# Optimization experiments

Measured on AMD Instinct MI355X. Metric: run time of the kernel, lower is better.

The kernel has to match this reference:

```python
import jax, jax.numpy as jnp
import numpy as np

B, N, C = 8, 2048, 128
K = 16
DILATIONS = (1, 2)
KMAX = K * max(DILATIONS)  # neighbors constructed by DilatedKnnGraph
NEG_SLOPE = 0.2


def setup_inputs() -> dict:
    key = jax.random.key(0)
    ks = jax.random.split(key, 12)
    D = len(DILATIONS)

    def nrm(k, shape, fan_in):
        return jax.random.normal(k, shape, jnp.float32) / np.float32(np.sqrt(fan_in))

    x = jax.random.normal(ks[0], (B, N, C), jnp.float32)
    pos = jax.random.normal(ks[1], (B, N, 3), jnp.float32)
    # PointTransformerConv params per dilation layer (bias-free lin/lin_src/lin_dst, pos_nn=Linear(3,C))
    W_lin = nrm(ks[2], (D, C, C), C)
    W_src = nrm(ks[3], (D, C, C), C)
    W_dst = nrm(ks[4], (D, C, C), C)
    W_pos = nrm(ks[5], (D, 3, C), 3)
    b_pos = jnp.zeros((D, C), jnp.float32)
    # global fusion MLP: Linear(C+3, C) + LeakyReLU(0.2)
    Wg = nrm(ks[6], (C + 3, C), C + 3)
    bg = jnp.zeros((C,), jnp.float32)
    # final MLP: Linear(C,C) + LeakyReLU(0.2) + Linear(C,3)
    W1 = nrm(ks[7], (C, C), C)
    b1 = jnp.zeros((C,), jnp.float32)
    W2 = nrm(ks[8], (C, 3), C)
    b2 = jnp.zeros((3,), jnp.float32)
    return dict(x=x, pos=pos, W_lin=W_lin, W_src=W_src, W_dst=W_dst,
                W_pos=W_pos, b_pos=b_pos, Wg=Wg, bg=bg, W1=W1, b1=b1, W2=W2, b2=b2)


def _knn(p):
    # p: [N, 3] -> [N, KMAX] neighbor indices sorted by ascending distance (self excluded)
    sq = jnp.sum(p * p, axis=-1)
    d2 = sq[:, None] + sq[None, :] - 2.0 * (p @ p.T)
    d2 = d2 + jnp.eye(p.shape[0], dtype=p.dtype) * jnp.float32(1e10)
    _, idx = jax.lax.top_k(-d2, KMAX)
    return idx


def reference(x, pos, W_lin, W_src, W_dst, W_pos, b_pos, Wg, bg, W1, b1, W2, b2):
    nbr = jax.vmap(_knn)(pos)  # [B, N, KMAX]
    self_idx = jnp.broadcast_to(jnp.arange(N)[None, :, None], (B, N, 1))
    gather = jax.vmap(lambda arr, idx: arr[idx])  # per-cloud fancy gather

    h = None
    for li, d in enumerate(DILATIONS):
        # Dilated neighbor selection: every d-th of sorted neighbors, keep K, plus self loop
        idx = jnp.concatenate([nbr[:, :, ::d][:, :, :K], self_idx], axis=-1)  # [B, N, K+1]
        pos_j = gather(pos, idx)  # [B, N, K+1, 3]
        # delta_ij = pos_nn(pos_i - pos_j)
        delta = jnp.einsum('bnkt,tc->bnkc', pos[:, :, None, :] - pos_j, W_pos[li]) + b_pos[li]
        s = x @ W_src[li]   # lin_src
        v = x @ W_lin[li]   # value projection
        t = x @ W_dst[li]   # lin_dst
        # alpha_ij = lin_dst(x_i) - lin_src(x_j) + delta ; per-channel softmax over neighbors
        alpha = t[:, :, None, :] - gather(s, idx) + delta  # [B, N, K+1, C]
        w = jax.nn.softmax(alpha, axis=2)
        h_ = jnp.sum(w * (gather(v, idx) + delta), axis=2)  # [B, N, C]
        h = h_ if h is None else h + h_

    h2 = jax.nn.leaky_relu(jnp.concatenate([x, pos], axis=-1) @ Wg + bg, NEG_SLOPE)
    h = h + h2
    res = jax.nn.leaky_relu(h @ W1 + b1, NEG_SLOPE) @ W2 + b2
    return res + pos  # add_points=True
```

## Files before the change

### kernel.cpp

```cpp
#include <hip/hip_runtime.h>

#define BB 8
#define NN 2048
#define CC 128
#define KMAX 32
#define NEG 0.2f
#define CH 8
#define CHSZ (NN / CH)
#define CPAD4 257
#define CAP 32

using bf16x8 = __attribute__((ext_vector_type(8))) short;
using f32x4  = __attribute__((ext_vector_type(4))) float;

__device__ __forceinline__ unsigned int f2key(float f) {
  unsigned int b = __float_as_uint(f);
  return (b & 0x80000000u) ? ~b : (b | 0x80000000u);
}

__device__ __forceinline__ float sq3(float x, float y, float z) {
  return __fadd_rn(__fadd_rn(__fmul_rn(x, x), __fmul_rn(y, y)), __fmul_rn(z, z));
}

__device__ __forceinline__ float d2np(float px, float py, float pz, float sqq,
                                      float qx, float qy, float qz, float sqj) {
  float dot = __fmaf_rn(pz, qz, __fmaf_rn(py, qy, __fmul_rn(px, qx)));
  return __fsub_rn(__fadd_rn(sqq, sqj), __fmul_rn(2.0f, dot));
}

__device__ __forceinline__ unsigned short f2bf(float f) {
  unsigned int u = __float_as_uint(f);
  return (unsigned short)((u + 0x7fffu + ((u >> 16) & 1u)) >> 16);
}
__device__ __forceinline__ float bf2f(unsigned short u) {
  return __uint_as_float(((unsigned int)u) << 16);
}

__device__ __forceinline__ bf16x8 cvt8(const float* __restrict__ p) {
  float4 a = *(const float4*)(p);
  float4 b = *(const float4*)(p + 4);
  bf16x8 r;
  r[0] = (short)f2bf(a.x); r[1] = (short)f2bf(a.y);
  r[2] = (short)f2bf(a.z); r[3] = (short)f2bf(a.w);
  r[4] = (short)f2bf(b.x); r[5] = (short)f2bf(b.y);
  r[6] = (short)f2bf(b.z); r[7] = (short)f2bf(b.w);
  return r;
}

__device__ __forceinline__ void proj_body(int z, int mx, int tid,
                                          const float* __restrict__ x,
                                          const unsigned short* __restrict__ wf,
                                          unsigned short* __restrict__ projb) {
  unsigned short* out = projb + (size_t)z * ((size_t)BB * NN * CC);
  int wave = tid >> 6;
  int lane = tid & 63;
  int m0 = (mx * 4 + wave) * 16;
  int quad = lane >> 4;
  int am = m0 + (lane & 15);

  f32x4 acc[8];
#pragma unroll
  for (int nt = 0; nt < 8; ++nt) acc[nt] = (f32x4){0.f, 0.f, 0.f, 0.f};

  const unsigned short* wz = wf + (size_t)z * (8 * 4 * 64 * 8);
#pragma unroll
  for (int ks = 0; ks < 4; ++ks) {
    bf16x8 a = cvt8(x + (size_t)am * CC + ks * 32 + quad * 8);
#pragma unroll
    for (int nt = 0; nt < 8; ++nt) {
      bf16x8 bfr = *(const bf16x8*)(wz + (size_t)(((nt * 4 + ks) * 64 + lane) * 8));
      acc[nt] = __builtin_amdgcn_mfma_f32_16x16x32_bf16(a, bfr, acc[nt], 0, 0, 0);
    }
  }

  int col0 = lane & 15;
#pragma unroll
  for (int nt = 0; nt < 8; ++nt)
#pragma unroll
    for (int r = 0; r < 4; ++r)
      out[(size_t)(m0 + quad * 4 + r) * CC + nt * 16 + col0] = f2bf(acc[nt][r]);
}

__device__ __forceinline__ void wg_body(int mx, int tid,
                                        const float* __restrict__ x,
                                        const float* __restrict__ pos,
                                        const unsigned short* __restrict__ wf,
                                        const float* __restrict__ wgtail,
                                        const float* __restrict__ bg,
                                        float* __restrict__ h) {
  int wave = tid >> 6;
  int lane = tid & 63;
  int m0 = (mx * 4 + wave) * 16;
  int quad = lane >> 4;
  int am = m0 + (lane & 15);

  f32x4 acc[8];
#pragma unroll
  for (int nt = 0; nt < 8; ++nt) acc[nt] = (f32x4){0.f, 0.f, 0.f, 0.f};

  const unsigned short* wz = wf + (size_t)6 * (8 * 4 * 64 * 8);
#pragma unroll
  for (int ks = 0; ks < 4; ++ks) {
    bf16x8 a = cvt8(x + (size_t)am * CC + ks * 32 + quad * 8);
#pragma unroll
    for (int nt = 0; nt < 8; ++nt) {
      bf16x8 b = *(const bf16x8*)(wz + (size_t)(((nt * 4 + ks) * 64 + lane) * 8));
      acc[nt] = __builtin_amdgcn_mfma_f32_16x16x32_bf16(a, b, acc[nt], 0, 0, 0);
    }
  }

  float posr[4][3];
#pragma unroll
  for (int r = 0; r < 4; ++r) {
    int m = m0 + quad * 4 + r;
    posr[r][0] = pos[m * 3 + 0];
    posr[r][1] = pos[m * 3 + 1];
    posr[r][2] = pos[m * 3 + 2];
  }

  int col0 = lane & 15;
#pragma unroll
  for (int nt = 0; nt < 8; ++nt) {
    int col = nt * 16 + col0;
    float bv = bg[col];
    float t0 = wgtail[col];
    float t1 = wgtail[CC + col];
    float t2 = wgtail[2 * CC + col];
#pragma unroll
    for (int r = 0; r < 4; ++r) {
      float v = acc[nt][r] + bv
              + posr[r][0] * t0 + posr[r][1] * t1 + posr[r][2] * t2;
      v = v > 0.f ? v : NEG * v;
      h[(size_t)(m0 + quad * 4 + r) * CC + col] = v;
    }
  }
}

__global__ __launch_bounds__(256) void fused_front(
    const float* __restrict__ pos,
    unsigned short* __restrict__ cand,
    unsigned int* __restrict__ candk,
    const float* __restrict__ x,
    const unsigned short* __restrict__ wf,
    unsigned short* __restrict__ projb,
    const float* __restrict__ wgtail,
    const float* __restrict__ bg,
    float* __restrict__ h) {
  __shared__ float4 sp4[CH * CPAD4];
  __shared__ unsigned int sred[256];
  __shared__ unsigned short sbuf[256 * CAP];

  if (blockIdx.x < 512) {
    int b = blockIdx.x >> 6;
    int qbase = (blockIdx.x & 63) * 32;
    const float* pb = pos + (size_t)b * NN * 3;
    for (int t = threadIdx.x; t < NN; t += 256) {
      int a = ((t >> 8) * CPAD4) + (t & 255);
      float xx = pb[t * 3 + 0];
      float yy = pb[t * 3 + 1];
      float zz = pb[t * 3 + 2];
      sp4[a] = make_float4(xx, yy, zz, sq3(xx, yy, zz));
    }
    __syncthreads();

    int q = qbase + (threadIdx.x >> 3);
    int c = threadIdx.x & 7;
    int qa = ((q >> 8) * CPAD4) + (q & 255);
    float4 pq = sp4[qa];
    float px = pq.x, py = pq.y, pz = pq.z;
    float sqq = pq.w;

    int abase = c * CPAD4;
    int j0 = c * CHSZ;

    unsigned int a0 = 0xFFFFFFFFu, a1 = 0xFFFFFFFFu, a2 = 0xFFFFFFFFu, a3 = 0xFFFFFFFFu;
    for (int jj = 0; jj < CHSZ; ++jj) {
      int j = j0 + jj;
      float4 pj = sp4[abase + jj];
      float d2 = d2np(px, py, pz, sqq, pj.x, pj.y, pj.z, pj.w);
      unsigned int key = f2key(d2);
      if (j == q) key = 0xFFFFFFFFu;
      if (key < a3) {
        bool c3 = key < a2;
        a3 = c3 ? a2 : key;
        bool c2 = key < a1;
        a2 = c3 ? (c2 ? a1 : key) : a2;
        bool c1 = key < a0;
        a1 = c2 ? (c1 ? a0 : key) : a1;
        a0 = c1 ? key : a0;
      }
    }
    sred[threadIdx.x] = a3;
    __syncthreads();
    if (c == 0) {
      unsigned int m = sred[threadIdx.x];
#pragma unroll
      for (int u = 1; u < 8; ++u) {
        unsigned int v = sred[threadIdx.x + u];
        m = v > m ? v : m;
      }
      sred[threadIdx.x] = m;
    }
    __syncthreads();
    unsigned int T = sred[threadIdx.x & ~7];

    unsigned int ak[KMAX];
    int ai[KMAX];
#pragma unroll
    for (int k = 0; k < KMAX; ++k) { ak[k] = 0xFFFFFFFFu; ai[k] = 0xFFFF; }

    int sbase = threadIdx.x * CAP;
    auto drain = [&](int cnt2) {
      for (int u = 0; u < cnt2; ++u) {
        int jj2 = (int)sbuf[sbase + u];
        int j = j0 + jj2;
        float4 pj = sp4[abase + jj2];
        float d2 = d2np(px, py, pz, sqq, pj.x, pj.y, pj.z, pj.w);
        unsigned int key = f2key(d2);
        if (key < ak[KMAX - 1]) {
#pragma unroll
          for (int k = KMAX - 1; k >= 1; --k) {
            bool ck  = key < ak[k];
            bool ckm = key < ak[k - 1];
            unsigned int tk = ckm ? ak[k - 1] : key;
            int          ti = ckm ? ai[k - 1] : j;
            ak[k] = ck ? tk : ak[k];
            ai[k] = ck ? ti : ai[k];
          }
          bool c0b = key < ak[0];
          ak[0] = c0b ? key : ak[0];
          ai[0] = c0b ? j : ai[0];
        }
      }
    };

    int cnt = 0;
    for (int jj = 0; jj < CHSZ; ++jj) {
      int j = j0 + jj;
      float4 pj = sp4[abase + jj];
      float d2 = d2np(px, py, pz, sqq, pj.x, pj.y, pj.z, pj.w);
      unsigned int key = f2key(d2);
      if (j == q) key = 0xFFFFFFFFu;
      if (key <= T) {
        if (cnt == CAP) { drain(CAP); cnt = 0; }
        sbuf[sbase + cnt] = (unsigned short)jj;
        ++cnt;
      }
    }
    drain(cnt);

    size_t obase = (((size_t)(b * NN + q)) * CH + c) * KMAX;
    unsigned short* oc = cand + obase;
    unsigned int* ok = candk + obase;
#pragma unroll
    for (int k = 0; k < KMAX; ++k) {
      oc[k] = (unsigned short)ai[k];
      ok[k] = ak[k];
    }
  } else if (blockIdx.x < 2048) {
    int bx = blockIdx.x - 512;
    proj_body(bx >> 8, bx & 255, threadIdx.x, x, wf, projb);
  } else {
    wg_body(blockIdx.x - 2048, threadIdx.x, x, pos, wf, wgtail, bg, h);
  }
}

__global__ __launch_bounds__(256) void knn_p1(const float* __restrict__ pos,
                                              unsigned short* __restrict__ cand,
                                              unsigned int* __restrict__ candk) {
  __shared__ float4 sp4[CH * CPAD4];
  __shared__ unsigned int sred[256];
  __shared__ unsigned short sbuf[256 * CAP];
  int b = blockIdx.x >> 6;
  int qbase = (blockIdx.x & 63) * 32;
  const float* pb = pos + (size_t)b * NN * 3;
  for (int t = threadIdx.x; t < NN; t += 256) {
    int a = ((t >> 8) * CPAD4) + (t & 255);
    float xx = pb[t * 3 + 0];
    float yy = pb[t * 3 + 1];
    float zz = pb[t * 3 + 2];
    sp4[a] = make_float4(xx, yy, zz, sq3(xx, yy, zz));
  }
  __syncthreads();

  int q = qbase + (threadIdx.x >> 3);
  int c = threadIdx.x & 7;
  int qa = ((q >> 8) * CPAD4) + (q & 255);
  float4 pq = sp4[qa];
  float px = pq.x, py = pq.y, pz = pq.z;
  float sqq = pq.w;

  int abase = c * CPAD4;
  int j0 = c * CHSZ;

  unsigned int a0 = 0xFFFFFFFFu, a1 = 0xFFFFFFFFu, a2 = 0xFFFFFFFFu, a3 = 0xFFFFFFFFu;
  for (int jj = 0; jj < CHSZ; ++jj) {
    int j = j0 + jj;
    float4 pj = sp4[abase + jj];
    float d2 = d2np(px, py, pz, sqq, pj.x, pj.y, pj.z, pj.w);
    unsigned int key = f2key(d2);
    if (j == q) key = 0xFFFFFFFFu;
    if (key < a3) {
      bool c3 = key < a2;
      a3 = c3 ? a2 : key;
      bool c2 = key < a1;
      a2 = c3 ? (c2 ? a1 : key) : a2;
      bool c1 = key < a0;
      a1 = c2 ? (c1 ? a0 : key) : a1;
      a0 = c1 ? key : a0;
    }
  }
  sred[threadIdx.x] = a3;
  __syncthreads();
  if (c == 0) {
    unsigned int m = sred[threadIdx.x];
#pragma unroll
    for (int u = 1; u < 8; ++u) {
      unsigned int v = sred[threadIdx.x + u];
      m = v > m ? v : m;
    }
    sred[threadIdx.x] = m;
  }
  __syncthreads();
  unsigned int T = sred[threadIdx.x & ~7];

  unsigned int ak[KMAX];
  int ai[KMAX];
#pragma unroll
  for (int k = 0; k < KMAX; ++k) { ak[k] = 0xFFFFFFFFu; ai[k] = 0xFFFF; }

  int sbase = threadIdx.x * CAP;
  auto drain = [&](int cnt2) {
    for (int u = 0; u < cnt2; ++u) {
      int jj2 = (int)sbuf[sbase + u];
      int j = j0 + jj2;
      float4 pj = sp4[abase + jj2];
      float d2 = d2np(px, py, pz, sqq, pj.x, pj.y, pj.z, pj.w);
      unsigned int key = f2key(d2);
      if (key < ak[KMAX - 1]) {
#pragma unroll
        for (int k = KMAX - 1; k >= 1; --k) {
          bool ck  = key < ak[k];
          bool ckm = key < ak[k - 1];
          unsigned int tk = ckm ? ak[k - 1] : key;
          int          ti = ckm ? ai[k - 1] : j;
          ak[k] = ck ? tk : ak[k];
          ai[k] = ck ? ti : ai[k];
        }
        bool c0b = key < ak[0];
        ak[0] = c0b ? key : ak[0];
        ai[0] = c0b ? j : ai[0];
      }
    }
  };

  int cnt = 0;
  for (int jj = 0; jj < CHSZ; ++jj) {
    int j = j0 + jj;
    float4 pj = sp4[abase + jj];
    float d2 = d2np(px, py, pz, sqq, pj.x, pj.y, pj.z, pj.w);
    unsigned int key = f2key(d2);
    if (j == q) key = 0xFFFFFFFFu;
    if (key <= T) {
      if (cnt == CAP) { drain(CAP); cnt = 0; }
      sbuf[sbase + cnt] = (unsigned short)jj;
      ++cnt;
    }
  }
  drain(cnt);

  size_t obase = (((size_t)(b * NN + q)) * CH + c) * KMAX;
  unsigned short* oc = cand + obase;
  unsigned int* ok = candk + obase;
#pragma unroll
  for (int k = 0; k < KMAX; ++k) {
    oc[k] = (unsigned short)ai[k];
    ok[k] = ak[k];
  }
}

__global__ __launch_bounds__(64) void knn_p2(const unsigned int* __restrict__ candk,
                                             const unsigned short* __restrict__ cand,
                                             int* __restrict__ nbr) {
  int q = blockIdx.x * 64 + threadIdx.x;
  const unsigned int* k8 = candk + (size_t)q * (CH * KMAX);
  const unsigned short* i8 = cand + (size_t)q * (CH * KMAX);

  int head[CH];
  unsigned int hk[CH];
#pragma unroll
  for (int c = 0; c < CH; ++c) {
    head[c] = 0;
    hk[c] = k8[c * KMAX];
  }

  int* onb = nbr + (size_t)q * KMAX;
#pragma unroll
  for (int r = 0; r < KMAX; ++r) {
    int bc = 0;
    unsigned int bk = hk[0];
#pragma unroll
    for (int c = 1; c < CH; ++c) {
      if (hk[c] < bk) { bk = hk[c]; bc = c; }
    }
    onb[r] = (int)i8[bc * KMAX + head[bc]];
    ++head[bc];
    hk[bc] = (head[bc] < KMAX) ? k8[bc * KMAX + head[bc]] : 0xFFFFFFFFu;
  }
}

__global__ __launch_bounds__(256) void wcvt(const float* __restrict__ Wa,
                                            const float* __restrict__ Wb,
                                            const float* __restrict__ Wc,
                                            const float* __restrict__ Wgm,
                                            const float* __restrict__ W1m,
                                            unsigned short* __restrict__ wf) {
  int t = blockIdx.x * 256 + threadIdx.x;
  int lane = t & 63;
  int ks = (t >> 6) & 3;
  int nt = (t >> 8) & 7;
  int z = t >> 11;
  const float* W = (z < 2) ? (Wa + (size_t)z * CC * CC)
                 : (z < 4) ? (Wb + (size_t)(z - 2) * CC * CC)
                 : (z < 6) ? (Wc + (size_t)(z - 4) * CC * CC)
                 : (z == 6) ? Wgm : W1m;
  int n = nt * 16 + (lane & 15);
  int kb = ks * 32 + (lane >> 4) * 8;
  unsigned short* o = wf + (size_t)t * 8;
#pragma unroll
  for (int j = 0; j < 8; ++j)
    o[j] = f2bf(W[(size_t)(kb + j) * CC + n]);
}

__global__ __launch_bounds__(256) void proj_fly(const float* __restrict__ x,
                                                const unsigned short* __restrict__ wf,
                                                unsigned short* __restrict__ projb) {
  proj_body(blockIdx.z, blockIdx.x, threadIdx.x, x, wf, projb);
}
__global__ __launch_bounds__(256) void wg_fly(const float* __restrict__ x,
                                              const float* __restrict__ pos,
                                              const unsigned short* __restrict__ wf,
                                              const float* __restrict__ wgtail,
                                              const float* __restrict__ bg,
                                              float* __restrict__ h) {
  wg_body(blockIdx.x, threadIdx.x, x, pos, wf, wgtail, bg, h);
}

__global__ __launch_bounds__(128) void attn2_kernel(
    const float* __restrict__ pos, const int* __restrict__ nbr,
    const unsigned short* __restrict__ s0, const unsigned short* __restrict__ v0,
    const unsigned short* __restrict__ t0,
    const unsigned short* __restrict__ s1, const unsigned short* __restrict__ v1,
    const unsigned short* __restrict__ t1,
    const float* __restrict__ Wpos, const float* __restrict__ bpos,
    const float* __restrict__ h, unsigned short* __restrict__ hb) {
  int b = blockIdx.x & 7;
  int n = blockIdx.x >> 3;
  int bn = (b << 11) + n;
  int c = threadIdx.x;

  const float* pb = pos + (size_t)b * NN * 3;
  float pix = pb[n * 3 + 0], piy = pb[n * 3 + 1], piz = pb[n * 3 + 2];
  const int* nb = nbr + (size_t)bn * KMAX;

  float ht = h[(size_t)bn * CC + c];

#pragma unroll
  for (int l = 0; l < 2; ++l) {
    int dil = l + 1;
    const unsigned short* s = l ? s1 : s0;
    const unsigned short* v = l ? v1 : v0;
    const unsigned short* t = l ? t1 : t0;
    const float* Wp = Wpos + (size_t)l * 3 * CC;
    float w0 = Wp[c], w1 = Wp[CC + c], w2 = Wp[2 * CC + c];
    float bp = bpos[(size_t)l * CC + c];
    float tc = bf2f(t[(size_t)bn * CC + c]);

    float alpha[17], del[17];
    float mx = -1e30f;
#pragma unroll
    for (int j = 0; j < 17; ++j) {
      int idx = (j < 16) ? nb[j * dil] : n;
      float dx = pix - pb[idx * 3 + 0];
      float dy = piy - pb[idx * 3 + 1];
      float dz = piz - pb[idx * 3 + 2];
      float d = dx * w0 + dy * w1 + dz * w2 + bp;
      del[j] = d;
      float sc = bf2f(s[((size_t)(b * NN + idx)) * CC + c]);
      float a = tc - sc + d;
      alpha[j] = a;
      mx = fmaxf(mx, a);
    }
    float sum = 0.f;
#pragma unroll
    for (int j = 0; j < 17; ++j) {
      float w = __expf(alpha[j] - mx);
      alpha[j] = w;
      sum += w;
    }
    float inv = 1.f / sum;
    float hc = 0.f;
#pragma unroll
    for (int j = 0; j < 17; ++j) {
      int idx = (j < 16) ? nb[j * dil] : n;
      float vc = bf2f(v[((size_t)(b * NN + idx)) * CC + c]);
      hc += alpha[j] * (vc + del[j]);
    }
    ht += hc * inv;
  }

  hb[(size_t)bn * CC + c] = f2bf(ht);
}

__global__ __launch_bounds__(256) void mfma_w1_final(
    const unsigned short* __restrict__ hb,
    const unsigned short* __restrict__ wz,
    const float* __restrict__ b1,
    const float* __restrict__ W2,
    const float* __restrict__ b2,
    const float* __restrict__ pos,
    float* __restrict__ out) {
  int wave = threadIdx.x >> 6;
  int lane = threadIdx.x & 63;
  int m0 = (blockIdx.x * 4 + wave) * 16;
  int quad = lane >> 4;
  int am = m0 + (lane & 15);

  f32x4 acc[8];
#pragma unroll
  for (int nt = 0; nt < 8; ++nt) acc[nt] = (f32x4){0.f, 0.f, 0.f, 0.f};

#pragma unroll
  for (int ks = 0; ks < 4; ++ks) {
    bf16x8 a = *(const bf16x8*)(hb + (size_t)am * CC + ks * 32 + quad * 8);
#pragma unroll
    for (int nt = 0; nt < 8; ++nt) {
      bf16x8 b = *(const bf16x8*)(wz + (size_t)(((nt * 4 + ks) * 64 + lane) * 8));
      acc[nt] = __builtin_amdgcn_mfma_f32_16x16x32_bf16(a, b, acc[nt], 0, 0, 0);
    }
  }

  int col0 = lane & 15;
  float part[4][3];
#pragma unroll
  for (int r = 0; r < 4; ++r)
#pragma unroll
    for (int d = 0; d < 3; ++d) part[r][d] = 0.f;

#pragma unroll
  for (int nt = 0; nt < 8; ++nt) {
    int col = nt * 16 + col0;
    float bv = b1[col];
    float w20 = W2[col * 3 + 0];
    float w21 = W2[col * 3 + 1];
    float w22 = W2[col * 3 + 2];
#pragma unroll
    for (int r = 0; r < 4; ++r) {
      float gv = acc[nt][r] + bv;
      gv = gv > 0.f ? gv : NEG * gv;
      part[r][0] = fmaf(gv, w20, part[r][0]);
      part[r][1] = fmaf(gv, w21, part[r][1]);
      part[r][2] = fmaf(gv, w22, part[r][2]);
    }
  }

#pragma unroll
  for (int off = 8; off >= 1; off >>= 1) {
#pragma unroll
    for (int r = 0; r < 4; ++r)
#pragma unroll
      for (int d = 0; d < 3; ++d)
        part[r][d] += __shfl_xor(part[r][d], off);
  }

  if (col0 == 0) {
#pragma unroll
    for (int r = 0; r < 4; ++r) {
      int m = m0 + quad * 4 + r;
#pragma unroll
      for (int d = 0; d < 3; ++d)
        out[(size_t)m * 3 + d] = part[r][d] + b2[d] + pos[(size_t)m * 3 + d];
    }
  }
}

extern "C" void kernel_launch(void* const* d_in, const int* in_sizes, int n_in,
                              void* d_out, int out_size, void* d_ws, size_t ws_size,
                              hipStream_t stream) {
  const float* x     = (const float*)d_in[0];
  const float* pos   = (const float*)d_in[1];
  const float* W_lin = (const float*)d_in[2];
  const float* W_src = (const float*)d_in[3];
  const float* W_dst = (const float*)d_in[4];
  const float* W_pos = (const float*)d_in[5];
  const float* b_pos = (const float*)d_in[6];
  const float* Wg    = (const float*)d_in[7];
  const float* bg    = (const float*)d_in[8];
  const float* W1    = (const float*)d_in[9];
  const float* b1    = (const float*)d_in[10];
  const float* W2    = (const float*)d_in[11];
  const float* b2    = (const float*)d_in[12];
  float* out = (float*)d_out;

  const size_t M = (size_t)BB * NN;
  const size_t MC = M * CC;

  char* ws = (char*)d_ws;
  int* nbr = (int*)ws;
  unsigned short* cand = (unsigned short*)(ws + M * KMAX * sizeof(int));
  float* fb = (float*)(ws + M * KMAX * sizeof(int) + M * CH * KMAX * sizeof(unsigned short));
  unsigned short* projb = (unsigned short*)fb;
  unsigned short* sb0 = projb + 0 * MC;
  unsigned short* sb1 = projb + 1 * MC;
  unsigned short* vb0 = projb + 2 * MC;
  unsigned short* vb1 = projb + 3 * MC;
  unsigned short* tb0 = projb + 4 * MC;
  unsigned short* tb1 = projb + 5 * MC;
  unsigned int* candk = (unsigned int*)(fb + 3 * MC);
  float* h = fb + 5 * MC;

  const size_t BASE = M * KMAX * sizeof(int) + M * CH * KMAX * sizeof(unsigned short)
                    + 8 * MC * sizeof(float);
  const size_t XB_BYTES = MC * sizeof(unsigned short);
  const size_t WF_BYTES = 8 * 16384 * sizeof(unsigned short);
  const size_t FRAG = (size_t)(8 * 4 * 64 * 8);
  bool fused_ok = ws_size >= BASE + XB_BYTES + WF_BYTES;

  if (fused_ok) {
    unsigned short* hb = (unsigned short*)(ws + BASE);
    unsigned short* wf = (unsigned short*)(ws + BASE + XB_BYTES);

    wcvt<<<64, 256, 0, stream>>>(W_src, W_lin, W_dst, Wg, W1, wf);
    fused_front<<<2304, 256, 0, stream>>>(pos, cand, candk, x, wf, projb,
                                          Wg + 128 * CC, bg, h);
    knn_p2<<<256, 64, 0, stream>>>(candk, cand, nbr);
    attn2_kernel<<<M, 128, 0, stream>>>(pos, nbr, sb0, vb0, tb0,
                                        sb1, vb1, tb1, W_pos, b_pos, h, hb);
    mfma_w1_final<<<M / 64, 256, 0, stream>>>(hb, wf + 7 * FRAG, b1,
                                              W2, b2, pos, out);
  } else {
    unsigned short* hb = cand;
    unsigned short* wf = cand + MC;
    knn_p1<<<512, 256, 0, stream>>>(pos, cand, candk);
    knn_p2<<<256, 64, 0, stream>>>(candk, cand, nbr);
    wcvt<<<64, 256, 0, stream>>>(W_src, W_lin, W_dst, Wg, W1, wf);
    proj_fly<<<dim3(256, 1, 6), 256, 0, stream>>>(x, wf, projb);
    wg_fly<<<256, 256, 0, stream>>>(x, pos, wf, Wg + 128 * CC, bg, h);
    attn2_kernel<<<M, 128, 0, stream>>>(pos, nbr, sb0, vb0, tb0,
                                        sb1, vb1, tb1, W_pos, b_pos, h, hb);
    mfma_w1_final<<<M / 64, 256, 0, stream>>>(hb, wf + 7 * FRAG, b1,
                                              W2, b2, pos, out);
  }
}
```

Baseline: 232.3 us.

## Streamline kNN candidate pass with float min/max network, shuffles, and XOR-swizzled LDS

Moves the kNN first pass into a shared device function used by both the fused front kernel and knn_p1. The branchy top-4 insertion on integer keys becomes a branchless fminf/fmaxf network on floats. The shared-memory threshold reduction and its barriers become sub-wave xor shuffles. Position padding is replaced by an XOR swizzle, and the candidate buffer shrinks to bytes, cutting LDS use to allow more resident blocks. The float comparison with sentinel and the d2<=T filter must keep the same neighbor ordering as the integer-key version.

```diff
diff --git a/kernel.cpp b/kernel.cpp
--- a/kernel.cpp
+++ b/kernel.cpp
@@ -7,7 +7,6 @@
 #define NEG 0.2f
 #define CH 8
 #define CHSZ (NN / CH)
-#define CPAD4 257
 #define CAP 32
 
 using bf16x8 = __attribute__((ext_vector_type(8))) short;
@@ -45,6 +44,103 @@
   r[4] = (short)f2bf(b.x); r[5] = (short)f2bf(b.y);
   r[6] = (short)f2bf(b.z); r[7] = (short)f2bf(b.w);
   return r;
+}
+
+__device__ __forceinline__ int paddr(int c, int jj) { return (c << 8) + (jj ^ c); }
+
+__device__ __forceinline__ void knn_body(int bx, int tid,
+                                         const float* __restrict__ pos,
+                                         unsigned short* __restrict__ cand,
+                                         unsigned int* __restrict__ candk,
+                                         float4* __restrict__ sp4,
+                                         unsigned char* __restrict__ sbuf) {
+  int b = bx >> 6;
+  int qbase = (bx & 63) * 32;
+  const float* pb = pos + (size_t)b * NN * 3;
+  for (int t = tid; t < NN; t += 256) {
+    float xx = pb[t * 3 + 0];
+    float yy = pb[t * 3 + 1];
+    float zz = pb[t * 3 + 2];
+    sp4[paddr(t >> 8, t & 255)] = make_float4(xx, yy, zz, sq3(xx, yy, zz));
+  }
+  __syncthreads();
+
+  int q = qbase + (tid >> 3);
+  int c = tid & 7;
+  float4 pq = sp4[paddr(q >> 8, q & 255)];
+  float px = pq.x, py = pq.y, pz = pq.z;
+  float sqq = pq.w;
+  int j0 = c * CHSZ;
+
+  const float SENT = 3.0e38f;
+  float a0 = SENT, a1 = SENT, a2 = SENT, a3 = SENT;
+#pragma unroll 4
+  for (int jj = 0; jj < CHSZ; ++jj) {
+    float4 pj = sp4[paddr(c, jj)];
+    float d2 = d2np(px, py, pz, sqq, pj.x, pj.y, pj.z, pj.w);
+    if (j0 + jj == q) d2 = SENT;
+    float m0 = fmaxf(a0, d2); a0 = fminf(a0, d2);
+    float m1 = fmaxf(a1, m0); a1 = fminf(a1, m0);
+    float m2 = fmaxf(a2, m1); a2 = fminf(a2, m1);
+    a3 = fminf(a3, m2);
+  }
+
+  float T = a3;
+  T = fmaxf(T, __shfl_xor(T, 1));
+  T = fmaxf(T, __shfl_xor(T, 2));
+  T = fmaxf(T, __shfl_xor(T, 4));
+
+  unsigned int ak[KMAX];
+  int ai[KMAX];
+#pragma unroll
+  for (int k = 0; k < KMAX; ++k) { ak[k] = 0xFFFFFFFFu; ai[k] = 0xFFFF; }
+
+  int sbase = tid * CAP;
+  auto drain = [&](int cnt2) {
+    for (int u = 0; u < cnt2; ++u) {
+      int jj2 = (int)sbuf[sbase + u];
+      int j = j0 + jj2;
+      float4 pj = sp4[paddr(c, jj2)];
+      float d2 = d2np(px, py, pz, sqq, pj.x, pj.y, pj.z, pj.w);
+      unsigned int key = f2key(d2);
+      if (key < ak[KMAX - 1]) {
+#pragma unroll
+        for (int k = KMAX - 1; k >= 1; --k) {
+          bool ck  = key < ak[k];
+          bool ckm = key < ak[k - 1];
+          unsigned int tk = ckm ? ak[k - 1] : key;
+          int          ti = ckm ? ai[k - 1] : j;
+          ak[k] = ck ? tk : ak[k];
+          ai[k] = ck ? ti : ai[k];
+        }
+        bool c0b = key < ak[0];
+        ak[0] = c0b ? key : ak[0];
+        ai[0] = c0b ? j : ai[0];
+      }
+    }
+  };
+
+  int cnt = 0;
+  for (int jj = 0; jj < CHSZ; ++jj) {
+    float4 pj = sp4[paddr(c, jj)];
+    float d2 = d2np(px, py, pz, sqq, pj.x, pj.y, pj.z, pj.w);
+    bool pass = (d2 <= T) && (j0 + jj != q);
+    if (pass) {
+      if (cnt == CAP) { drain(CAP); cnt = 0; }
+      sbuf[sbase + cnt] = (unsigned char)jj;
+      ++cnt;
+    }
+  }
+  drain(cnt);
+
+  size_t obase = (((size_t)(b * NN + q)) * CH + c) * KMAX;
+  unsigned short* oc = cand + obase;
+  unsigned int* ok = candk + obase;
+#pragma unroll
+  for (int k = 0; k < KMAX; ++k) {
+    oc[k] = (unsigned short)ai[k];
+    ok[k] = ak[k];
+  }
 }
 
 __device__ __forceinline__ void proj_body(int z, int mx, int tid,
@@ -146,117 +242,11 @@
     const float* __restrict__ wgtail,
     const float* __restrict__ bg,
     float* __restrict__ h) {
-  __shared__ float4 sp4[CH * CPAD4];
-  __shared__ unsigned int sred[256];
-  __shared__ unsigned short sbuf[256 * CAP];
+  __shared__ float4 sp4[CH * 256];
+  __shared__ unsigned char sbuf[256 * CAP];
 
   if (blockIdx.x < 512) {
-    int b = blockIdx.x >> 6;
-    int qbase = (blockIdx.x & 63) * 32;
-    const float* pb = pos + (size_t)b * NN * 3;
-    for (int t = threadIdx.x; t < NN; t += 256) {
-      int a = ((t >> 8) * CPAD4) + (t & 255);
-      float xx = pb[t * 3 + 0];
-      float yy = pb[t * 3 + 1];
-      float zz = pb[t * 3 + 2];
-      sp4[a] = make_float4(xx, yy, zz, sq3(xx, yy, zz));
-    }
-    __syncthreads();
-
-    int q = qbase + (threadIdx.x >> 3);
-    int c = threadIdx.x & 7;
-    int qa = ((q >> 8) * CPAD4) + (q & 255);
-    float4 pq = sp4[qa];
-    float px = pq.x, py = pq.y, pz = pq.z;
-    float sqq = pq.w;
-
-    int abase = c * CPAD4;
-    int j0 = c * CHSZ;
-
-    unsigned int a0 = 0xFFFFFFFFu, a1 = 0xFFFFFFFFu, a2 = 0xFFFFFFFFu, a3 = 0xFFFFFFFFu;
-    for (int jj = 0; jj < CHSZ; ++jj) {
-      int j = j0 + jj;
-      float4 pj = sp4[abase + jj];
-      float d2 = d2np(px, py, pz, sqq, pj.x, pj.y, pj.z, pj.w);
-      unsigned int key = f2key(d2);
-      if (j == q) key = 0xFFFFFFFFu;
-      if (key < a3) {
-        bool c3 = key < a2;
-        a3 = c3 ? a2 : key;
-        bool c2 = key < a1;
-        a2 = c3 ? (c2 ? a1 : key) : a2;
-        bool c1 = key < a0;
-        a1 = c2 ? (c1 ? a0 : key) : a1;
-        a0 = c1 ? key : a0;
-      }
-    }
-    sred[threadIdx.x] = a3;
-    __syncthreads();
-    if (c == 0) {
-      unsigned int m = sred[threadIdx.x];
-#pragma unroll
-      for (int u = 1; u < 8; ++u) {
-        unsigned int v = sred[threadIdx.x + u];
-        m = v > m ? v : m;
-      }
-      sred[threadIdx.x] = m;
-    }
-    __syncthreads();
-    unsigned int T = sred[threadIdx.x & ~7];
-
-    unsigned int ak[KMAX];
-    int ai[KMAX];
-#pragma unroll
-    for (int k = 0; k < KMAX; ++k) { ak[k] = 0xFFFFFFFFu; ai[k] = 0xFFFF; }
-
-    int sbase = threadIdx.x * CAP;
-    auto drain = [&](int cnt2) {
-      for (int u = 0; u < cnt2; ++u) {
-        int jj2 = (int)sbuf[sbase + u];
-        int j = j0 + jj2;
-        float4 pj = sp4[abase + jj2];
-        float d2 = d2np(px, py, pz, sqq, pj.x, pj.y, pj.z, pj.w);
-        unsigned int key = f2key(d2);
-        if (key < ak[KMAX - 1]) {
-#pragma unroll
-          for (int k = KMAX - 1; k >= 1; --k) {
-            bool ck  = key < ak[k];
-            bool ckm = key < ak[k - 1];
-            unsigned int tk = ckm ? ak[k - 1] : key;
-            int          ti = ckm ? ai[k - 1] : j;
-            ak[k] = ck ? tk : ak[k];
-            ai[k] = ck ? ti : ai[k];
-          }
-          bool c0b = key < ak[0];
-          ak[0] = c0b ? key : ak[0];
-          ai[0] = c0b ? j : ai[0];
-        }
-      }
-    };
-
-    int cnt = 0;
-    for (int jj = 0; jj < CHSZ; ++jj) {
-      int j = j0 + jj;
-      float4 pj = sp4[abase + jj];
-      float d2 = d2np(px, py, pz, sqq, pj.x, pj.y, pj.z, pj.w);
-      unsigned int key = f2key(d2);
-      if (j == q) key = 0xFFFFFFFFu;
-      if (key <= T) {
-        if (cnt == CAP) { drain(CAP); cnt = 0; }
-        sbuf[sbase + cnt] = (unsigned short)jj;
-        ++cnt;
-      }
-    }
-    drain(cnt);
-
-    size_t obase = (((size_t)(b * NN + q)) * CH + c) * KMAX;
-    unsigned short* oc = cand + obase;
-    unsigned int* ok = candk + obase;
-#pragma unroll
-    for (int k = 0; k < KMAX; ++k) {
-      oc[k] = (unsigned short)ai[k];
-      ok[k] = ak[k];
-    }
+    knn_body(blockIdx.x, threadIdx.x, pos, cand, candk, sp4, sbuf);
   } else if (blockIdx.x < 2048) {
     int bx = blockIdx.x - 512;
     proj_body(bx >> 8, bx & 255, threadIdx.x, x, wf, projb);
@@ -268,115 +258,9 @@
 __global__ __launch_bounds__(256) void knn_p1(const float* __restrict__ pos,
                                               unsigned short* __restrict__ cand,
                                               unsigned int* __restrict__ candk) {
-  __shared__ float4 sp4[CH * CPAD4];
-  __shared__ unsigned int sred[256];
-  __shared__ unsigned short sbuf[256 * CAP];
-  int b = blockIdx.x >> 6;
-  int qbase = (blockIdx.x & 63) * 32;
-  const float* pb = pos + (size_t)b * NN * 3;
-  for (int t = threadIdx.x; t < NN; t += 256) {
-    int a = ((t >> 8) * CPAD4) + (t & 255);
-    float xx = pb[t * 3 + 0];
-    float yy = pb[t * 3 + 1];
-    float zz = pb[t * 3 + 2];
-    sp4[a] = make_float4(xx, yy, zz, sq3(xx, yy, zz));
-  }
-  __syncthreads();
-
-  int q = qbase + (threadIdx.x >> 3);
-  int c = threadIdx.x & 7;
-  int qa = ((q >> 8) * CPAD4) + (q & 255);
-  float4 pq = sp4[qa];
-  float px = pq.x, py = pq.y, pz = pq.z;
-  float sqq = pq.w;
-
-  int abase = c * CPAD4;
-  int j0 = c * CHSZ;
-
-  unsigned int a0 = 0xFFFFFFFFu, a1 = 0xFFFFFFFFu, a2 = 0xFFFFFFFFu, a3 = 0xFFFFFFFFu;
-  for (int jj = 0; jj < CHSZ; ++jj) {
-    int j = j0 + jj;
-    float4 pj = sp4[abase + jj];
-    float d2 = d2np(px, py, pz, sqq, pj.x, pj.y, pj.z, pj.w);
-    unsigned int key = f2key(d2);
-    if (j == q) key = 0xFFFFFFFFu;
-    if (key < a3) {
-      bool c3 = key < a2;
-      a3 = c3 ? a2 : key;
-      bool c2 = key < a1;
-      a2 = c3 ? (c2 ? a1 : key) : a2;
-      bool c1 = key < a0;
-      a1 = c2 ? (c1 ? a0 : key) : a1;
-      a0 = c1 ? key : a0;
-    }
-  }
-  sred[threadIdx.x] = a3;
-  __syncthreads();
-  if (c == 0) {
-    unsigned int m = sred[threadIdx.x];
-#pragma unroll
-    for (int u = 1; u < 8; ++u) {
-      unsigned int v = sred[threadIdx.x + u];
-      m = v > m ? v : m;
-    }
-    sred[threadIdx.x] = m;
-  }
-  __syncthreads();
-  unsigned int T = sred[threadIdx.x & ~7];
-
-  unsigned int ak[KMAX];
-  int ai[KMAX];
-#pragma unroll
-  for (int k = 0; k < KMAX; ++k) { ak[k] = 0xFFFFFFFFu; ai[k] = 0xFFFF; }
-
-  int sbase = threadIdx.x * CAP;
-  auto drain = [&](int cnt2) {
-    for (int u = 0; u < cnt2; ++u) {
-      int jj2 = (int)sbuf[sbase + u];
-      int j = j0 + jj2;
-      float4 pj = sp4[abase + jj2];
-      float d2 = d2np(px, py, pz, sqq, pj.x, pj.y, pj.z, pj.w);
-      unsigned int key = f2key(d2);
-      if (key < ak[KMAX - 1]) {
-#pragma unroll
-        for (int k = KMAX - 1; k >= 1; --k) {
-          bool ck  = key < ak[k];
-          bool ckm = key < ak[k - 1];
-          unsigned int tk = ckm ? ak[k - 1] : key;
-          int          ti = ckm ? ai[k - 1] : j;
-          ak[k] = ck ? tk : ak[k];
-          ai[k] = ck ? ti : ai[k];
-        }
-        bool c0b = key < ak[0];
-        ak[0] = c0b ? key : ak[0];
-        ai[0] = c0b ? j : ai[0];
-      }
-    }
-  };
-
-  int cnt = 0;
-  for (int jj = 0; jj < CHSZ; ++jj) {
-    int j = j0 + jj;
-    float4 pj = sp4[abase + jj];
-    float d2 = d2np(px, py, pz, sqq, pj.x, pj.y, pj.z, pj.w);
-    unsigned int key = f2key(d2);
-    if (j == q) key = 0xFFFFFFFFu;
-    if (key <= T) {
-      if (cnt == CAP) { drain(CAP); cnt = 0; }
-      sbuf[sbase + cnt] = (unsigned short)jj;
-      ++cnt;
-    }
-  }
-  drain(cnt);
-
-  size_t obase = (((size_t)(b * NN + q)) * CH + c) * KMAX;
-  unsigned short* oc = cand + obase;
-  unsigned int* ok = candk + obase;
-#pragma unroll
-  for (int k = 0; k < KMAX; ++k) {
-    oc[k] = (unsigned short)ai[k];
-    ok[k] = ak[k];
-  }
+  __shared__ float4 sp4[CH * 256];
+  __shared__ unsigned char sbuf[256 * CAP];
+  knn_body(blockIdx.x, threadIdx.x, pos, cand, candk, sp4, sbuf);
 }
 
 __global__ __launch_bounds__(64) void knn_p2(const unsigned int* __restrict__ candk,
```

Measured after the change: 218.2 us. -6.1%, faster.
